# Optimization experiments

Measured on AMD Instinct MI355X. Metric: run time of the kernel, lower is better.

Reference implementation:

```python
import jax, jax.numpy as jnp
import numpy as np

H_DIM = 256
N_HEADS = 8
HEAD_DIM = H_DIM // N_HEADS
B, N = 2, 2048
LN_EPS = 1e-5


def setup_inputs() -> dict:
    key = jax.random.key(0)
    ks = jax.random.split(key, 20)
    s = 1.0 / np.sqrt(H_DIM)
    inp = {
        'hidden': jax.random.normal(ks[0], (B, N, H_DIM), jnp.float32),
        'adjacency': jax.random.uniform(ks[1], (B, N, N), jnp.float32),
        'positions': jax.random.uniform(ks[2], (B, N, 2), jnp.float32),
        # linear weights stored as (in, out): y = x @ W + b
        'wq': jax.random.normal(ks[3], (H_DIM, H_DIM), jnp.float32) * s,
        'bq': jnp.zeros((H_DIM,), jnp.float32),
        'wk': jax.random.normal(ks[4], (H_DIM, H_DIM), jnp.float32) * s,
        'bk': jnp.zeros((H_DIM,), jnp.float32),
        'wv': jax.random.normal(ks[5], (H_DIM, H_DIM), jnp.float32) * s,
        'bv': jnp.zeros((H_DIM,), jnp.float32),
        'wo': jax.random.normal(ks[6], (H_DIM, H_DIM), jnp.float32) * s,
        'bo': jnp.zeros((H_DIM,), jnp.float32),
        'g1': jnp.ones((H_DIM,), jnp.float32),
        'b1': jnp.zeros((H_DIM,), jnp.float32),
        'g2': jnp.ones((H_DIM,), jnp.float32),
        'b2': jnp.zeros((H_DIM,), jnp.float32),
        'w_ff1': jax.random.normal(ks[7], (H_DIM, 4 * H_DIM), jnp.float32) * s,
        'b_ff1': jnp.zeros((4 * H_DIM,), jnp.float32),
        'w_ff2': jax.random.normal(ks[8], (4 * H_DIM, H_DIM), jnp.float32) * (1.0 / np.sqrt(4 * H_DIM)),
        'b_ff2': jnp.zeros((H_DIM,), jnp.float32),
    }
    return inp


def _layernorm(x, g, b):
    mu = jnp.mean(x, axis=-1, keepdims=True)
    var = jnp.var(x, axis=-1, keepdims=True)
    return (x - mu) * jax.lax.rsqrt(var + LN_EPS) * g + b


def reference(hidden, adjacency, positions, wq, bq, wk, bk, wv, bv, wo, bo,
              g1, b1, g2, b2, w_ff1, b_ff1, w_ff2, b_ff2):
    b_, n_, _ = hidden.shape
    normalized = _layernorm(hidden, g1, b1)
    # project and split heads: [B, H, N, Dh]
    def heads(x):
        return x.reshape(b_, n_, N_HEADS, HEAD_DIM).transpose(0, 2, 1, 3)
    q = heads(normalized @ wq + bq)
    k = heads(normalized @ wk + bk)
    v = heads(normalized @ wv + bv)
    logits = jnp.einsum('bhnd,bhmd->bhnm', q, k) / np.sqrt(HEAD_DIM)
    cond = adjacency[:, None, :, :]  # mode == 'connectivity'
    logits = logits + (2.0 * cond - 1.0)
    weights = jax.nn.softmax(logits, axis=-1)
    weights = weights * (0.25 + 0.75 * cond)
    weights = weights / jnp.maximum(weights.sum(axis=-1, keepdims=True), 1e-6)
    attended = jnp.einsum('bhnm,bhmd->bhnd', weights, v)
    attended = attended.transpose(0, 2, 1, 3).reshape(b_, n_, H_DIM)
    hidden = hidden + attended @ wo + bo
    h2 = _layernorm(hidden, g2, b2)
    ff = jax.nn.gelu(h2 @ w_ff1 + b_ff1, approximate=False) @ w_ff2 + b_ff2
    return hidden + ff
```

## Files before the change

### kernel.cpp

```cpp
#include <hip/hip_runtime.h>
#include <math.h>

#define BB 2
#define NN 2048
#define HD 256
#define NH 8
#define DH 32
#define NTOK (BB*NN)
#define QKVLD 768
#define NSPLIT 2
#define KVPB (NN/NSPLIT)
#define NTILES (KVPB/64)

typedef _Float16 h8 __attribute__((ext_vector_type(8)));
typedef _Float16 h4 __attribute__((ext_vector_type(4)));
typedef float fx4 __attribute__((ext_vector_type(4)));

#define LOG2E 1.4426950408889634f
#define SQ_LOG2 0.25503486f
#define C1A (2.0f * LOG2E)
#define C0A (-(LOG2E + 6.0f))

__device__ __forceinline__ void ln_row(const float* __restrict__ x,
    const float* __restrict__ g, const float* __restrict__ bta,
    _Float16* __restrict__ yh, int row, int lane)
{
  const float* xr = x + (size_t)row * HD + lane * 4;
  float4 v = *(const float4*)xr;
  float s = v.x + v.y + v.z + v.w;
  #pragma unroll
  for (int off = 32; off > 0; off >>= 1) s += __shfl_xor(s, off);
  float mu = s * (1.0f / HD);
  float dx0 = v.x - mu, dx1 = v.y - mu, dx2 = v.z - mu, dx3 = v.w - mu;
  float ss = dx0*dx0 + dx1*dx1 + dx2*dx2 + dx3*dx3;
  #pragma unroll
  for (int off = 32; off > 0; off >>= 1) ss += __shfl_xor(ss, off);
  float rinv = rsqrtf(ss * (1.0f / HD) + 1e-5f);
  float4 gv = *(const float4*)(g   + lane * 4);
  float4 bv = *(const float4*)(bta + lane * 4);
  h4 hh;
  hh[0] = (_Float16)(dx0 * rinv * gv.x + bv.x);
  hh[1] = (_Float16)(dx1 * rinv * gv.y + bv.y);
  hh[2] = (_Float16)(dx2 * rinv * gv.z + bv.z);
  hh[3] = (_Float16)(dx3 * rinv * gv.w + bv.w);
  *(h4*)(yh + (size_t)row * HD + lane * 4) = hh;
}

__global__ __launch_bounds__(256) void ln_kernel(const float* __restrict__ x,
    const float* __restrict__ g, const float* __restrict__ bta,
    _Float16* __restrict__ yh)
{
  ln_row(x, g, bta, yh, blockIdx.x * 4 + (threadIdx.x >> 6), threadIdx.x & 63);
}

__device__ __forceinline__ void do_transpose(const float* __restrict__ W,
    _Float16* __restrict__ Wh, int Nw, int rowoff, int ldout, float scale,
    int bx, int by, float (*tile)[33])
{
  int k0 = by * 32, n0 = bx * 32;
  int c = threadIdx.x & 31, r = threadIdx.x >> 5;
  #pragma unroll
  for (int i = 0; i < 4; i++)
    tile[r + i * 8][c] = W[(size_t)(k0 + r + i * 8) * Nw + n0 + c];
  __syncthreads();
  #pragma unroll
  for (int i = 0; i < 4; i++) {
    int n = r + i * 8;
    Wh[(size_t)(rowoff + n0 + n) * ldout + k0 + c] = (_Float16)(tile[c][n] * scale);
  }
}

__global__ __launch_bounds__(256) void prep_kernel(
    const float* wq, const float* wk, const float* wv, const float* wo,
    const float* wf1, const float* wf2,
    const float* bq, const float* bk, const float* bv,
    const float* hidden, const float* g1, const float* b1,
    _Float16* WtQKVh, _Float16* WtOh, _Float16* WtF1h, _Float16* WtF2h,
    float* biasqkv, _Float16* norm1h)
{
  __shared__ float tile[32][33];
  int bid = blockIdx.x;
  if (bid < 64)        do_transpose(wq,  WtQKVh,  256,   0,  256, SQ_LOG2, bid & 7, bid >> 3, tile);
  else if (bid < 128)  do_transpose(wk,  WtQKVh,  256, 256,  256, 1.0f, (bid-64) & 7, (bid-64) >> 3, tile);
  else if (bid < 192)  do_transpose(wv,  WtQKVh,  256, 512,  256, 1.0f, (bid-128) & 7, (bid-128) >> 3, tile);
  else if (bid < 256)  do_transpose(wo,  WtOh,    256,   0,  256, 1.0f, (bid-192) & 7, (bid-192) >> 3, tile);
  else if (bid < 512)  do_transpose(wf1, WtF1h,  1024,   0,  256, 1.0f, (bid-256) & 31, (bid-256) >> 5, tile);
  else if (bid < 768)  do_transpose(wf2, WtF2h,   256,   0, 1024, 1.0f, (bid-512) & 7, (bid-512) >> 3, tile);
  else if (bid == 768) {
    #pragma unroll
    for (int j = 0; j < 3; j++) {
      int t = j * 256 + threadIdx.x;
      biasqkv[t] = (t < 256) ? bq[t] * SQ_LOG2 : (t < 512) ? bk[t - 256] : bv[t - 512];
    }
  } else {
    ln_row(hidden, g1, b1, norm1h, (bid - 769) * 4 + (threadIdx.x >> 6), threadIdx.x & 63);
  }
}

template<int KK, int NT, int NX, int ACT, int RES, int OM>
__global__ __launch_bounds__(256) void gemm16_kernel(
    const _Float16* __restrict__ Ah, const _Float16* __restrict__ Wh,
    const float* __restrict__ bias, const float* __restrict__ resid,
    float* __restrict__ Cf, _Float16* __restrict__ Ch,
    _Float16* __restrict__ vtb, int N)
{
  const int lin = blockIdx.x;
  const int qch = gridDim.x >> 3;
  const int wg = (lin & 7) * qch + (lin >> 3);
  const int bx = wg % NX, by = wg / NX;
  const int n0 = bx * (NT * 16);
  const int m0 = by * 64;
  const int t = threadIdx.x, w = t >> 6, l = t & 63;
  const int ml = l & 15, g = l >> 4;
  const int mrow = m0 + w * 16 + ml;

  const _Float16* aph = Ah + (size_t)mrow * KK + g * 8;
  const _Float16* whp[NT];
  #pragma unroll
  for (int nt = 0; nt < NT; nt++)
    whp[nt] = Wh + (size_t)(n0 + nt * 16 + ml) * KK + g * 8;

  fx4 acc[NT];
  #pragma unroll
  for (int nt = 0; nt < NT; nt++) acc[nt] = (fx4){0.f, 0.f, 0.f, 0.f};

  #pragma unroll 4
  for (int k0 = 0; k0 < KK; k0 += 32) {
    h8 ah = *(const h8*)(aph + k0);
    #pragma unroll
    for (int nt = 0; nt < NT; nt++) {
      h8 wh = *(const h8*)(whp[nt] + k0);
      acc[nt] = __builtin_amdgcn_mfma_f32_16x16x32_f16(ah, wh, acc[nt], 0, 0, 0);
    }
  }

  #pragma unroll
  for (int nt = 0; nt < NT; nt++) {
    int n = n0 + nt * 16 + ml;
    float bv = bias[n];
    #pragma unroll
    for (int i = 0; i < 4; i++) {
      int m = m0 + w * 16 + 4 * g + i;
      float vv = acc[nt][i] + bv;
      if (ACT == 1) vv = 0.5f * vv * (1.0f + erff(vv * 0.70710678118654752f));
      if (RES)      vv += resid[(size_t)m * N + n];
      if (OM == 0) {
        Cf[(size_t)m * N + n] = vv;
      } else if (OM == 1) {
        Ch[(size_t)m * N + n] = (_Float16)vv;
      } else {
        if (n < 512) Ch[(size_t)m * QKVLD + n] = (_Float16)vv;
        else {
          int dim = n - 512, kv = m & (NN - 1), bb = m >> 11;
          int kvp = (kv & ~31) | ((kv & 15) << 1) | ((kv >> 4) & 1);
          vtb[((size_t)(bb * HD + dim)) * NN + kvp] = (_Float16)vv;
        }
      }
    }
  }
}

__global__ __launch_bounds__(256) void wo_fused_kernel(
    const _Float16* __restrict__ Opart, const float* __restrict__ Spart,
    const _Float16* __restrict__ Wh, const float* __restrict__ bias,
    const float* __restrict__ resid, float* __restrict__ Cf)
{
  const int lin = blockIdx.x;
  const int qch = gridDim.x >> 3;
  const int wg = (lin & 7) * qch + (lin >> 3);
  const int bx = wg & 7, by = wg >> 3;
  const int n0 = bx * 32;
  const int m0 = by * 64;
  const int t = threadIdx.x, w = t >> 6, l = t & 63;
  const int ml = l & 15, g = l >> 4;
  const int mrow = m0 + w * 16 + ml;
  const int bb = mrow >> 11, qrow = mrow & (NN - 1);

  const _Float16* whp0 = Wh + (size_t)(n0 + ml) * HD + g * 8;
  const _Float16* whp1 = Wh + (size_t)(n0 + 16 + ml) * HD + g * 8;

  fx4 acc0 = {0.f, 0.f, 0.f, 0.f};
  fx4 acc1 = {0.f, 0.f, 0.f, 0.f};

  #pragma unroll
  for (int h = 0; h < NH; h++) {
    size_t p0 = ((size_t)((bb * 2 + 0) * NH + h)) * NN + qrow;
    size_t p1 = ((size_t)((bb * 2 + 1) * NH + h)) * NN + qrow;
    float s0 = Spart[p0], s1 = Spart[p1];
    float den = 1.0f / (s0 + s1);
    float w0 = s0 * den, w1 = s1 * den;
    h8 o0 = *(const h8*)(Opart + p0 * 32 + g * 8);
    h8 o1 = *(const h8*)(Opart + p1 * 32 + g * 8);
    h8 ah;
    #pragma unroll
    for (int j = 0; j < 8; j++)
      ah[j] = (_Float16)(w0 * (float)o0[j] + w1 * (float)o1[j]);
    h8 wh0 = *(const h8*)(whp0 + h * 32);
    h8 wh1 = *(const h8*)(whp1 + h * 32);
    acc0 = __builtin_amdgcn_mfma_f32_16x16x32_f16(ah, wh0, acc0, 0, 0, 0);
    acc1 = __builtin_amdgcn_mfma_f32_16x16x32_f16(ah, wh1, acc1, 0, 0, 0);
  }

  #pragma unroll
  for (int i = 0; i < 4; i++) {
    int m = m0 + w * 16 + 4 * g + i;
    int na = n0 + ml, nb = n0 + 16 + ml;
    Cf[(size_t)m * HD + na] = acc0[i] + bias[na] + resid[(size_t)m * HD + na];
    Cf[(size_t)m * HD + nb] = acc1[i] + bias[nb] + resid[(size_t)m * HD + nb];
  }
}

__global__ __launch_bounds__(512) void attn_mfma_kernel(
    const _Float16* __restrict__ qkv16, const _Float16* __restrict__ vtb,
    const float* __restrict__ adj,
    _Float16* __restrict__ Opart, float* __restrict__ Spart)
{
  __shared__ _Float16 Ksh[2][2][64][40];
  __shared__ _Float16 Vp[2][2][32][72];
  __shared__ _Float16 AdjL[2][64][68];

  const int z = blockIdx.z;
  const int b = z >> 1, half = z & 1;
  const int hg = blockIdx.y;
  const int q0 = blockIdx.x * 64;
  const int t = threadIdx.x;
  const int hh_ = t >> 8;
  const int head = hg * 2 + hh_;
  const int tl = t & 255;
  const int w = tl >> 6, l = t & 63;
  const int m = l & 15, g = l >> 4;
  const int kvbase = half * KVPB;

  const int qrow = q0 + w * 16 + m;
  h8 qh = *(const h8*)(qkv16 + ((size_t)(b * NN + qrow)) * QKVLD + head * DH + g * 8);

  fx4 ot0 = {0.f, 0.f, 0.f, 0.f};
  fx4 ot1 = {0.f, 0.f, 0.f, 0.f};
  float S4[4] = {0.f, 0.f, 0.f, 0.f};

  const int arow0 = t >> 4;
  const int acol = (t & 15) * 4;
  const float* adjbase = adj + ((size_t)(b * NN + q0)) * NN + kvbase;

  const int krow = tl >> 2, kd0 = (tl & 3) * 8;
  const int vdim = tl >> 3, vkc = (tl & 7) * 8;
  const _Float16* kbase = qkv16 + ((size_t)(b * NN + kvbase + krow)) * QKVLD + 256 + head * DH + kd0;
  const _Float16* vbase = vtb + ((size_t)(b * HD + head * DH + vdim)) * NN + kvbase + vkc;

  h8 kreg = *(const h8*)kbase;
  h8 vreg = *(const h8*)vbase;

  {
    float4 ar[2];
    #pragma unroll
    for (int j = 0; j < 2; j++)
      ar[j] = *(const float4*)(adjbase + (size_t)(j * 32 + arow0) * NN + acol);
    #pragma unroll
    for (int j = 0; j < 2; j++) {
      h4 hh;
      hh[0] = (_Float16)ar[j].x; hh[1] = (_Float16)ar[j].y;
      hh[2] = (_Float16)ar[j].z; hh[3] = (_Float16)ar[j].w;
      *(h4*)&AdjL[0][j * 32 + arow0][acol] = hh;
    }
  }
  *(h8*)&Ksh[hh_][0][krow][kd0] = kreg;
  *(h8*)&Vp[hh_][0][vdim][vkc]  = vreg;
  kreg = *(const h8*)(kbase + (size_t)64 * QKVLD);
  vreg = *(const h8*)(vbase + 64);
  __syncthreads();

  for (int tt = 0; tt < NTILES; ++tt) {
    const int cur = tt & 1;

    float4 ar[2];
    if (tt + 1 < NTILES) {
      #pragma unroll
      for (int j = 0; j < 2; j++)
        ar[j] = *(const float4*)(adjbase + (size_t)(j * 32 + arow0) * NN
                                 + (tt + 1) * 64 + acol);
    }

    h8 kh0 = *(const h8*)&Ksh[hh_][cur][     m][g * 8];
    h8 kh1 = *(const h8*)&Ksh[hh_][cur][16 + m][g * 8];
    h8 kh2 = *(const h8*)&Ksh[hh_][cur][32 + m][g * 8];
    h8 kh3 = *(const h8*)&Ksh[hh_][cur][48 + m][g * 8];
    fx4 z4 = {0.f, 0.f, 0.f, 0.f};
    fx4 st[4];
    st[0] = __builtin_amdgcn_mfma_f32_16x16x32_f16(kh0, qh, z4, 0, 0, 0);
    st[1] = __builtin_amdgcn_mfma_f32_16x16x32_f16(kh1, qh, z4, 0, 0, 0);
    st[2] = __builtin_amdgcn_mfma_f32_16x16x32_f16(kh2, qh, z4, 0, 0, 0);
    st[3] = __builtin_amdgcn_mfma_f32_16x16x32_f16(kh3, qh, z4, 0, 0, 0);

    float pv[16];
    #pragma unroll
    for (int p = 0; p < 4; p++) {
      h4 ah4 = *(const h4*)&AdjL[cur][w * 16 + m][p * 16 + g * 4];
      float ps = 0.f;
      #pragma unroll
      for (int i = 0; i < 4; i++) {
        float a = (float)ah4[i];
        float e = __builtin_amdgcn_exp2f(st[p][i] + C1A * a + C0A);
        float pp = (0.25f + 0.75f * a) * e;
        pv[p * 4 + i] = pp;
        ps += pp;
      }
      S4[p] += ps;
    }
    h8 ph0, ph1;
    #pragma unroll
    for (int q2 = 0; q2 < 4; q2++) {
      ph0[2*q2]     = (_Float16)pv[q2];
      ph0[2*q2 + 1] = (_Float16)pv[4 + q2];
      ph1[2*q2]     = (_Float16)pv[8 + q2];
      ph1[2*q2 + 1] = (_Float16)pv[12 + q2];
    }

    h8 v00 = *(const h8*)&Vp[hh_][cur][m][g * 8];
    h8 v01 = *(const h8*)&Vp[hh_][cur][m][32 + g * 8];
    h8 v10 = *(const h8*)&Vp[hh_][cur][16 + m][g * 8];
    h8 v11 = *(const h8*)&Vp[hh_][cur][16 + m][32 + g * 8];
    ot0 = __builtin_amdgcn_mfma_f32_16x16x32_f16(v00, ph0, ot0, 0, 0, 0);
    ot0 = __builtin_amdgcn_mfma_f32_16x16x32_f16(v01, ph1, ot0, 0, 0, 0);
    ot1 = __builtin_amdgcn_mfma_f32_16x16x32_f16(v10, ph0, ot1, 0, 0, 0);
    ot1 = __builtin_amdgcn_mfma_f32_16x16x32_f16(v11, ph1, ot1, 0, 0, 0);

    if (tt + 1 < NTILES) {
      #pragma unroll
      for (int j = 0; j < 2; j++) {
        h4 hh;
        hh[0] = (_Float16)ar[j].x; hh[1] = (_Float16)ar[j].y;
        hh[2] = (_Float16)ar[j].z; hh[3] = (_Float16)ar[j].w;
        *(h4*)&AdjL[cur ^ 1][j * 32 + arow0][acol] = hh;
      }
      *(h8*)&Ksh[hh_][cur ^ 1][krow][kd0] = kreg;
      *(h8*)&Vp[hh_][cur ^ 1][vdim][vkc]  = vreg;
      if (tt + 2 < NTILES) {
        kreg = *(const h8*)(kbase + (size_t)((tt + 2) * 64) * QKVLD);
        vreg = *(const h8*)(vbase + (tt + 2) * 64);
      }
    }
    __syncthreads();
  }

  float S = (S4[0] + S4[1]) + (S4[2] + S4[3]);
  S += __shfl_xor(S, 16);
  S += __shfl_xor(S, 32);

  float is = 1.0f / S;
  size_t prow = ((size_t)(z * NH + head)) * NN + qrow;
  _Float16* po = Opart + prow * 32;
  h4 o0h, o1h;
  #pragma unroll
  for (int j = 0; j < 4; j++) {
    o0h[j] = (_Float16)(ot0[j] * is);
    o1h[j] = (_Float16)(ot1[j] * is);
  }
  *(h4*)(po + 4 * g)      = o0h;
  *(h4*)(po + 16 + 4 * g) = o1h;
  if (g == 0) Spart[prow] = S;
}

extern "C" void kernel_launch(void* const* d_in, const int* in_sizes, int n_in,
                              void* d_out, int out_size, void* d_ws, size_t ws_size,
                              hipStream_t stream)
{
  const float* hidden    = (const float*)d_in[0];
  const float* adjacency = (const float*)d_in[1];
  const float* wq  = (const float*)d_in[3];
  const float* bq  = (const float*)d_in[4];
  const float* wk  = (const float*)d_in[5];
  const float* bk  = (const float*)d_in[6];
  const float* wv  = (const float*)d_in[7];
  const float* bv  = (const float*)d_in[8];
  const float* wo  = (const float*)d_in[9];
  const float* bo  = (const float*)d_in[10];
  const float* g1  = (const float*)d_in[11];
  const float* b1  = (const float*)d_in[12];
  const float* g2  = (const float*)d_in[13];
  const float* b2  = (const float*)d_in[14];
  const float* wf1 = (const float*)d_in[15];
  const float* bf1 = (const float*)d_in[16];
  const float* wf2 = (const float*)d_in[17];
  const float* bf2 = (const float*)d_in[18];
  float* out = (float*)d_out;

  char* base = (char*)d_ws;
  const size_t MB = 1024 * 1024;
  _Float16* norm1h = (_Float16*)(base);
  _Float16* qkv16  = (_Float16*)(base + 2*MB);
  _Float16* vtb    = (_Float16*)(base + 8*MB);
  float*    hid2   = (float*)(base + 12*MB);
  _Float16* Opart = (_Float16*)(base + 16*MB);
  _Float16* ffah  = (_Float16*)(base + 16*MB);
  float* Spart = (float*)(base + 25*MB);
  _Float16* wtb = (_Float16*)(base + 26*MB);
  _Float16* WtQKVh = wtb; wtb += 768 * 256;
  _Float16* WtOh   = wtb; wtb += 256 * 256;
  _Float16* WtF1h  = wtb; wtb += 1024 * 256;
  _Float16* WtF2h  = wtb; wtb += 256 * 1024;
  float* biasqkv = (float*)(base + 28*MB);

  prep_kernel<<<1793, 256, 0, stream>>>(wq, wk, wv, wo, wf1, wf2, bq, bk, bv,
      hidden, g1, b1, WtQKVh, WtOh, WtF1h, WtF2h, biasqkv, norm1h);

  gemm16_kernel<256, 4, 12, 0, 0, 2><<<768, 256, 0, stream>>>(
      norm1h, WtQKVh, biasqkv, nullptr, nullptr, qkv16, vtb, QKVLD);

  attn_mfma_kernel<<<dim3(NN / 64, NH / 2, BB * NSPLIT), 512, 0, stream>>>(
      qkv16, vtb, adjacency, Opart, Spart);

  wo_fused_kernel<<<512, 256, 0, stream>>>(
      Opart, Spart, WtOh, bo, hidden, hid2);

  ln_kernel<<<NTOK / 4, 256, 0, stream>>>(hid2, g2, b2, norm1h);

  gemm16_kernel<256, 4, 16, 1, 0, 1><<<1024, 256, 0, stream>>>(
      norm1h, WtF1h, bf1, nullptr, nullptr, ffah, nullptr, 1024);

  gemm16_kernel<1024, 2, 8, 0, 1, 0><<<512, 256, 0, stream>>>(
      ffah, WtF2h, bf2, hid2, out, nullptr, nullptr, 256);
}
```

Measured before the change: 117.2 us.

## Process four heads per attention block with single-buffered LDS and prefetch GEMM operands

After: 118.1 us. About the same (+0.7%).

```diff
diff --git a/kernel.cpp b/kernel.cpp
--- a/kernel.cpp
+++ b/kernel.cpp
@@ -124,14 +124,26 @@
   #pragma unroll
   for (int nt = 0; nt < NT; nt++) acc[nt] = (fx4){0.f, 0.f, 0.f, 0.f};
 
-  #pragma unroll 4
-  for (int k0 = 0; k0 < KK; k0 += 32) {
-    h8 ah = *(const h8*)(aph + k0);
-    #pragma unroll
-    for (int nt = 0; nt < NT; nt++) {
-      h8 wh = *(const h8*)(whp[nt] + k0);
-      acc[nt] = __builtin_amdgcn_mfma_f32_16x16x32_f16(ah, wh, acc[nt], 0, 0, 0);
-    }
+  h8 ah = *(const h8*)(aph);
+  h8 wh[NT];
+  #pragma unroll
+  for (int nt = 0; nt < NT; nt++) wh[nt] = *(const h8*)(whp[nt]);
+
+  #pragma unroll 2
+  for (int k0 = 32; k0 <= KK; k0 += 32) {
+    h8 ahn;
+    h8 whn[NT];
+    if (k0 < KK) {
+      ahn = *(const h8*)(aph + k0);
+      #pragma unroll
+      for (int nt = 0; nt < NT; nt++) whn[nt] = *(const h8*)(whp[nt] + k0);
+    }
+    #pragma unroll
+    for (int nt = 0; nt < NT; nt++)
+      acc[nt] = __builtin_amdgcn_mfma_f32_16x16x32_f16(ah, wh[nt], acc[nt], 0, 0, 0);
+    ah = ahn;
+    #pragma unroll
+    for (int nt = 0; nt < NT; nt++) wh[nt] = whn[nt];
   }
 
   #pragma unroll
@@ -210,14 +222,14 @@
   }
 }
 
-__global__ __launch_bounds__(512) void attn_mfma_kernel(
+__global__ __launch_bounds__(1024) void attn_mfma_kernel(
     const _Float16* __restrict__ qkv16, const _Float16* __restrict__ vtb,
     const float* __restrict__ adj,
     _Float16* __restrict__ Opart, float* __restrict__ Spart)
 {
-  __shared__ _Float16 Ksh[2][2][64][40];
-  __shared__ _Float16 Vp[2][2][32][72];
-  __shared__ _Float16 AdjL[2][64][68];
+  __shared__ _Float16 Ksh[4][64][40];
+  __shared__ _Float16 Vp[4][32][72];
+  __shared__ _Float16 AdjL[64][68];
 
   const int z = blockIdx.z;
   const int b = z >> 1, half = z & 1;
@@ -225,7 +237,7 @@
   const int q0 = blockIdx.x * 64;
   const int t = threadIdx.x;
   const int hh_ = t >> 8;
-  const int head = hg * 2 + hh_;
+  const int head = hg * 4 + hh_;
   const int tl = t & 255;
   const int w = tl >> 6, l = t & 63;
   const int m = l & 15, g = l >> 4;
@@ -238,7 +250,7 @@
   fx4 ot1 = {0.f, 0.f, 0.f, 0.f};
   float S4[4] = {0.f, 0.f, 0.f, 0.f};
 
-  const int arow0 = t >> 4;
+  const int arow = t >> 4;
   const int acol = (t & 15) * 4;
   const float* adjbase = adj + ((size_t)(b * NN + q0)) * NN + kvbase;
 
@@ -249,41 +261,29 @@
 
   h8 kreg = *(const h8*)kbase;
   h8 vreg = *(const h8*)vbase;
-
-  {
-    float4 ar[2];
-    #pragma unroll
-    for (int j = 0; j < 2; j++)
-      ar[j] = *(const float4*)(adjbase + (size_t)(j * 32 + arow0) * NN + acol);
-    #pragma unroll
-    for (int j = 0; j < 2; j++) {
+  float4 areg = *(const float4*)(adjbase + (size_t)arow * NN + acol);
+
+  for (int tt = 0; tt < NTILES; ++tt) {
+    *(h8*)&Ksh[hh_][krow][kd0] = kreg;
+    *(h8*)&Vp[hh_][vdim][vkc]  = vreg;
+    {
       h4 hh;
-      hh[0] = (_Float16)ar[j].x; hh[1] = (_Float16)ar[j].y;
-      hh[2] = (_Float16)ar[j].z; hh[3] = (_Float16)ar[j].w;
-      *(h4*)&AdjL[0][j * 32 + arow0][acol] = hh;
-    }
-  }
-  *(h8*)&Ksh[hh_][0][krow][kd0] = kreg;
-  *(h8*)&Vp[hh_][0][vdim][vkc]  = vreg;
-  kreg = *(const h8*)(kbase + (size_t)64 * QKVLD);
-  vreg = *(const h8*)(vbase + 64);
-  __syncthreads();
-
-  for (int tt = 0; tt < NTILES; ++tt) {
-    const int cur = tt & 1;
-
-    float4 ar[2];
+      hh[0] = (_Float16)areg.x; hh[1] = (_Float16)areg.y;
+      hh[2] = (_Float16)areg.z; hh[3] = (_Float16)areg.w;
+      *(h4*)&AdjL[arow][acol] = hh;
+    }
+    __syncthreads();
+
     if (tt + 1 < NTILES) {
-      #pragma unroll
-      for (int j = 0; j < 2; j++)
-        ar[j] = *(const float4*)(adjbase + (size_t)(j * 32 + arow0) * NN
-                                 + (tt + 1) * 64 + acol);
-    }
-
-    h8 kh0 = *(const h8*)&Ksh[hh_][cur][     m][g * 8];
-    h8 kh1 = *(const h8*)&Ksh[hh_][cur][16 + m][g * 8];
-    h8 kh2 = *(const h8*)&Ksh[hh_][cur][32 + m][g * 8];
-    h8 kh3 = *(const h8*)&Ksh[hh_][cur][48 + m][g * 8];
+      kreg = *(const h8*)(kbase + (size_t)((tt + 1) * 64) * QKVLD);
+      vreg = *(const h8*)(vbase + (tt + 1) * 64);
+      areg = *(const float4*)(adjbase + (size_t)arow * NN + (tt + 1) * 64 + acol);
+    }
+
+    h8 kh0 = *(const h8*)&Ksh[hh_][     m][g * 8];
+    h8 kh1 = *(const h8*)&Ksh[hh_][16 + m][g * 8];
+    h8 kh2 = *(const h8*)&Ksh[hh_][32 + m][g * 8];
+    h8 kh3 = *(const h8*)&Ksh[hh_][48 + m][g * 8];
     fx4 z4 = {0.f, 0.f, 0.f, 0.f};
     fx4 st[4];
     st[0] = __builtin_amdgcn_mfma_f32_16x16x32_f16(kh0, qh, z4, 0, 0, 0);
@@ -294,7 +294,7 @@
     float pv[16];
     #pragma unroll
     for (int p = 0; p < 4; p++) {
-      h4 ah4 = *(const h4*)&AdjL[cur][w * 16 + m][p * 16 + g * 4];
+      h4 ah4 = *(const h4*)&AdjL[w * 16 + m][p * 16 + g * 4];
       float ps = 0.f;
       #pragma unroll
       for (int i = 0; i < 4; i++) {
@@ -315,30 +315,15 @@
       ph1[2*q2 + 1] = (_Float16)pv[12 + q2];
     }
 
-    h8 v00 = *(const h8*)&Vp[hh_][cur][m][g * 8];
-    h8 v01 = *(const h8*)&Vp[hh_][cur][m][32 + g * 8];
-    h8 v10 = *(const h8*)&Vp[hh_][cur][16 + m][g * 8];
-    h8 v11 = *(const h8*)&Vp[hh_][cur][16 + m][32 + g * 8];
+    h8 v00 = *(const h8*)&Vp[hh_][m][g * 8];
+    h8 v01 = *(const h8*)&Vp[hh_][m][32 + g * 8];
+    h8 v10 = *(const h8*)&Vp[hh_][16 + m][g * 8];
+    h8 v11 = *(const h8*)&Vp[hh_][16 + m][32 + g * 8];
     ot0 = __builtin_amdgcn_mfma_f32_16x16x32_f16(v00, ph0, ot0, 0, 0, 0);
     ot0 = __builtin_amdgcn_mfma_f32_16x16x32_f16(v01, ph1, ot0, 0, 0, 0);
     ot1 = __builtin_amdgcn_mfma_f32_16x16x32_f16(v10, ph0, ot1, 0, 0, 0);
     ot1 = __builtin_amdgcn_mfma_f32_16x16x32_f16(v11, ph1, ot1, 0, 0, 0);
 
-    if (tt + 1 < NTILES) {
-      #pragma unroll
-      for (int j = 0; j < 2; j++) {
-        h4 hh;
-        hh[0] = (_Float16)ar[j].x; hh[1] = (_Float16)ar[j].y;
-        hh[2] = (_Float16)ar[j].z; hh[3] = (_Float16)ar[j].w;
-        *(h4*)&AdjL[cur ^ 1][j * 32 + arow0][acol] = hh;
-      }
-      *(h8*)&Ksh[hh_][cur ^ 1][krow][kd0] = kreg;
-      *(h8*)&Vp[hh_][cur ^ 1][vdim][vkc]  = vreg;
-      if (tt + 2 < NTILES) {
-        kreg = *(const h8*)(kbase + (size_t)((tt + 2) * 64) * QKVLD);
-        vreg = *(const h8*)(vbase + (tt + 2) * 64);
-      }
-    }
     __syncthreads();
   }
 
@@ -406,7 +391,7 @@
   gemm16_kernel<256, 4, 12, 0, 0, 2><<<768, 256, 0, stream>>>(
       norm1h, WtQKVh, biasqkv, nullptr, nullptr, qkv16, vtb, QKVLD);
 
-  attn_mfma_kernel<<<dim3(NN / 64, NH / 2, BB * NSPLIT), 512, 0, stream>>>(
+  attn_mfma_kernel<<<dim3(NN / 64, NH / 4, BB * NSPLIT), 1024, 0, stream>>>(
       qkv16, vtb, adjacency, Opart, Spart);
 
   wo_fused_kernel<<<512, 256, 0, stream>>>(
```
